# Optimization experiments

Measured on AMD Instinct MI355X. Metric: run time of the kernel, lower is better.

The kernel has to match this reference:

```python
import jax, jax.numpy as jnp
import numpy as np
import math

EPS = jnp.float32(1.1920929e-07)      # torch.finfo(torch.float).eps
FMIN = jnp.finfo(jnp.float32).min     # torch.finfo(torch.float).min
NEG = jnp.float32(-1e9)


def setup_inputs() -> dict:
    key = jax.random.key(0)
    ks = jax.random.split(key, 9)
    bs, l, sub, tgt, hidden, t_vocab, voc = 16, 1024, 2, 256, 512, 2000, 3000
    return {
        "out_logits": jax.random.normal(ks[0], (bs, tgt, t_vocab), jnp.float32),
        "feature": jax.random.normal(ks[1], (bs, tgt, hidden), jnp.float32),
        "memory_raw": jax.random.normal(ks[2], (bs, l, hidden), jnp.float32),
        "content_e": jax.random.randint(ks[3], (bs, l * sub), 0, voc, jnp.int64
                                        if jax.config.jax_enable_x64 else jnp.int32),
        "Wq": jax.random.normal(ks[4], (hidden, hidden), jnp.float32) * 0.02,
        "bq": jax.random.normal(ks[5], (hidden,), jnp.float32) * 0.02,
        "Wk": jax.random.normal(ks[6], (hidden, hidden * sub), jnp.float32) * 0.02,
        "bk": jax.random.normal(ks[7], (hidden * sub,), jnp.float32) * 0.02,
        "sentinel": jax.random.uniform(ks[8], (1, hidden), jnp.float32),
        "voc_len": 3000,
    }


def reference(out_logits, feature, memory_raw, content_e, Wq, bq, Wk, bk, sentinel, voc_len):
    bs, l, hidden = memory_raw.shape
    tgt_len = feature.shape[1]
    subtokens = Wk.shape[1] // hidden
    src_len = l * subtokens

    # decode(): out = log_softmax(prob(feature)); key_linear + subtoken expansion
    out = jax.nn.log_softmax(out_logits, axis=-1)                     # (bs, t, t_vocab)
    memory = (memory_raw @ Wk + bk).reshape(bs, src_len, hidden)      # (bs, s, h)
    key_padding_mask = content_e == 0                                 # (bs, s)

    # pointer(): attention over memory + sentinel
    pointer_key = jnp.concatenate(
        [memory, jnp.broadcast_to(sentinel[None, :, :], (bs, 1, hidden))], axis=1)
    pointer_query = jax.nn.gelu(feature @ Wq + bq, approximate=False) # (bs, t, h)
    atten = jnp.einsum('bth,bsh->bts', pointer_query, pointer_key) / math.sqrt(hidden)

    mask = jnp.concatenate(
        [key_padding_mask, jnp.zeros((bs, 1), bool)], axis=-1)[:, None, :]
    atten = jnp.where(mask, NEG, atten)
    atten = jax.nn.log_softmax(atten, axis=-1)                        # (bs, t, s+1)

    pointer_gate = atten[:, :, -1:]                                   # (bs, t, 1)
    exp_atten = jnp.exp(atten[:, :, :-1])                             # (bs, t, s)

    # scatter-add over src positions by extended-vocab id (== one-hot M einsum)
    def scat(ea_b, ce_b):  # ea_b: (t, s)  ce_b: (s,)
        return jax.ops.segment_sum(ea_b.T, ce_b, num_segments=voc_len).T  # (t, voc)
    pointer_atten_p = jax.vmap(scat)(exp_atten, content_e)            # (bs, t, voc)

    pointer_atten_log = jnp.log(pointer_atten_p + EPS)
    pointer_atten_log = pointer_atten_log - jnp.log1p(-jnp.exp(pointer_gate) + EPS)
    pointer_atten_log = jnp.where(jnp.isneginf(pointer_atten_log), FMIN, pointer_atten_log)

    pad = jnp.full((bs, tgt_len, voc_len - out.shape[-1]), -jnp.inf, jnp.float32)
    out = jnp.concatenate([out, pad], axis=-1)                        # (bs, t, voc)

    p = jnp.stack([out + pointer_gate,
                   pointer_atten_log + jnp.log(1.0 - jnp.exp(pointer_gate) + EPS)],
                  axis=-2)                                            # (bs, t, 2, voc)
    return jax.scipy.special.logsumexp(p, axis=-2)                    # (bs, t, voc)
```

## Files before the change

### kernel.cpp

```cpp
#include <hip/hip_runtime.h>
#include <math.h>

#define BSZ   16
#define LSEQ  1024
#define TGT   256
#define HID   512
#define TV    2000
#define VOC   3000
#define SRC   2048
#define NKE   1280
#define JOFF  640
#define CTILE 256
#define SCALE 0.044194173824159216f

typedef unsigned short u16;
typedef __attribute__((ext_vector_type(8))) short bf16x8;
typedef __attribute__((ext_vector_type(4))) float f32x4;

__device__ __forceinline__ u16 f2bf(float x) {
    unsigned u = __float_as_uint(x);
    u += 0x7FFFu + ((u >> 16) & 1u);
    return (u16)(u >> 16);
}
__device__ __forceinline__ float bf2f(u16 x) {
    return __uint_as_float((unsigned)x << 16);
}

static __device__ __forceinline__ float gelu_exact(float x) {
    return 0.5f * x * (1.0f + erff(x * 0.70710678118654752f));
}

__device__ __forceinline__ void gload16(const u16* g, u16* l) {
    __builtin_amdgcn_global_load_lds(
        (const __attribute__((address_space(1))) unsigned int*)g,
        (__attribute__((address_space(3))) unsigned int*)l,
        16, 0, 0);
}

__device__ __forceinline__ void cast8_body(const float4* __restrict__ in,
                                           int4* __restrict__ out, int i) {
    float4 x = in[2 * i], y = in[2 * i + 1];
    unsigned p0 = (unsigned)f2bf(x.x) | ((unsigned)f2bf(x.y) << 16);
    unsigned p1 = (unsigned)f2bf(x.z) | ((unsigned)f2bf(x.w) << 16);
    unsigned p2 = (unsigned)f2bf(y.x) | ((unsigned)f2bf(y.y) << 16);
    unsigned p3 = (unsigned)f2bf(y.z) | ((unsigned)f2bf(y.w) << 16);
    out[i] = make_int4(p0, p1, p2, p3);
}

__global__ __launch_bounds__(256) void prep_a(
    const float* __restrict__ feature, const float* __restrict__ Wq,
    const float* __restrict__ Wk, const float* __restrict__ sentinel,
    const float* __restrict__ bk,
    int4* __restrict__ featb, u16* __restrict__ wqT, u16* __restrict__ wkE,
    float* __restrict__ rowsum)
{
    __shared__ float t[32][33];
    const int id = blockIdx.x;
    const int tid = threadIdx.x;
    if (id < 1024) {
        cast8_body((const float4*)feature, featb, id * 256 + tid);
    } else if (id < 1280) {
        int id2 = id - 1024;
        int bx = (id2 & 15) * 32, by = (id2 >> 4) * 32;
        const int tx = tid & 31, ty = tid >> 5;
        #pragma unroll
        for (int k = 0; k < 4; ++k)
            t[ty + 8 * k][tx] = Wq[(size_t)(by + ty + 8 * k) * 512 + bx + tx];
        __syncthreads();
        #pragma unroll
        for (int k = 0; k < 4; ++k)
            wqT[(size_t)(bx + ty + 8 * k) * 512 + by + tx] = f2bf(t[tx][ty + 8 * k]);
    } else if (id < 1600) {
        const int rr = (id - 1280) * 4 + (tid >> 6);
        const int c = (tid & 63) * 8;
        const int j = rr >= JOFF;
        const int dd = rr - j * JOFF;
        u16* dst = wkE + (size_t)rr * HID + c;
        if (dd < 512) {
            const float* src = Wk + (size_t)dd * 1024 + j * 512 + c;
            #pragma unroll
            for (int k = 0; k < 8; ++k) dst[k] = f2bf(src[k]);
        } else if (dd == 512) {
            #pragma unroll
            for (int k = 0; k < 8; ++k) dst[k] = f2bf(sentinel[c + k]);
        } else if (dd == 513) {
            #pragma unroll
            for (int k = 0; k < 8; ++k) dst[k] = f2bf(bk[j * 512 + c + k]);
        } else {
            #pragma unroll
            for (int k = 0; k < 8; ++k) dst[k] = 0;
        }
    } else {
        float4* rz = (float4*)rowsum;
        for (int i = tid; i < 1024; i += 256) rz[i] = make_float4(0.f, 0.f, 0.f, 0.f);
    }
}

__global__ __launch_bounds__(256) void k_query(
    const u16* __restrict__ feat, const u16* __restrict__ wqT,
    const float* __restrict__ bq, u16* __restrict__ queryb,
    const float* __restrict__ memory_raw, int4* __restrict__ memb)
{
    __shared__ u16 sbuf[2 * 2048 * 2];
    const int id = blockIdx.x;
    const int tid = threadIdx.x;
    if (id >= 512) {
        cast8_body((const float4*)memory_raw, memb, (id - 512) * 256 + tid);
        return;
    }
    u16* As = sbuf;
    u16* Bs = sbuf + 2 * 2048;
    const int lane = tid & 63;
    const int w = tid >> 6;
    const int wr = (w >> 1) * 32, wc = (w & 1) * 32;
    const int m0 = (id >> 3) * 64, n0 = (id & 7) * 64;

    const int srow = tid >> 2, scol = (tid & 3) * 8;
    const u16* gA = feat + (size_t)(m0 + srow) * HID + scol;
    const u16* gB = wqT + (size_t)(n0 + srow) * HID + scol;

    const int la = lane & 15, lb = lane >> 4;
    f32x4 acc[2][2] = {};

    gload16(gA, As + w * 512);
    gload16(gB, Bs + w * 512);

    int cur = 0;
    for (int k0 = 0; k0 < HID; k0 += 32) {
        __syncthreads();
        const u16* Asb = As + cur * 2048;
        const u16* Bsb = Bs + cur * 2048;
        bf16x8 af[2], bf[2];
        #pragma unroll
        for (int i = 0; i < 2; ++i)
            af[i] = *(const bf16x8*)(Asb + (wr + i * 16 + la) * 32 + lb * 8);
        #pragma unroll
        for (int j = 0; j < 2; ++j)
            bf[j] = *(const bf16x8*)(Bsb + (wc + j * 16 + la) * 32 + lb * 8);
        if (k0 + 32 < HID) {
            const int nb = cur ^ 1;
            gload16(gA + k0 + 32, As + nb * 2048 + w * 512);
            gload16(gB + k0 + 32, Bs + nb * 2048 + w * 512);
        }
        #pragma unroll
        for (int i = 0; i < 2; ++i)
            #pragma unroll
            for (int j = 0; j < 2; ++j)
                acc[i][j] = __builtin_amdgcn_mfma_f32_16x16x32_bf16(af[i], bf[j], acc[i][j], 0, 0, 0);
        cur ^= 1;
    }

    const int r_l = (lane >> 4) * 4, c_l = lane & 15;
    #pragma unroll
    for (int j = 0; j < 2; ++j) {
        const int n = n0 + wc + j * 16 + c_l;
        const float bv = bq[n];
        #pragma unroll
        for (int i = 0; i < 2; ++i)
            #pragma unroll
            for (int r = 0; r < 4; ++r) {
                const int m = m0 + wr + i * 16 + r_l + r;
                queryb[(size_t)m * HID + n] = f2bf(gelu_exact(acc[i][j][r] + bv));
            }
    }
}

template<int EPI, int LDA, int LDB>
__device__ __forceinline__ void gemm_body(
    int m0, int n0, int z,
    const u16* __restrict__ Abase, const u16* __restrict__ Bbase,
    u16* __restrict__ outb,
    const int* __restrict__ ce, float* __restrict__ rowsum,
    u16* __restrict__ As, u16* __restrict__ Bs)
{
    const int tid = threadIdx.x;
    const int lane = tid & 63;
    const int w = tid >> 6;
    const int wr = (w >> 1) * 64, wc = (w & 1) * 64;

    const u16* Ag = Abase;
    const u16* Bg = Bbase;
    if (EPI == 2) {
        Ag = Abase + (size_t)(z >> 1) * LSEQ * HID;
        Bg = Bbase + (size_t)(z >> 1) * TGT * NKE + (size_t)(z & 1) * JOFF;
    }

    const int chunkrow = lane >> 2;
    const int colc = (lane & 3) * 8;
    const int c0 = w * 2, c1 = c0 + 1;
    const u16* gA0 = Ag + (size_t)(m0 + c0 * 16 + chunkrow) * LDA + colc;
    const u16* gA1 = Ag + (size_t)(m0 + c1 * 16 + chunkrow) * LDA + colc;
    const u16* gB0 = Bg + (size_t)(n0 + c0 * 16 + chunkrow) * LDB + colc;
    const u16* gB1 = Bg + (size_t)(n0 + c1 * 16 + chunkrow) * LDB + colc;

    const int la = lane & 15, lb = lane >> 4;
    f32x4 acc[4][4] = {};

    gload16(gA0, As + c0 * 512);
    gload16(gA1, As + c1 * 512);
    gload16(gB0, Bs + c0 * 512);
    gload16(gB1, Bs + c1 * 512);

    int cur = 0;
    for (int k0 = 0; k0 < HID; k0 += 32) {
        __syncthreads();
        const u16* Asb = As + cur * 4096;
        const u16* Bsb = Bs + cur * 4096;
        bf16x8 af[4], bfv[4];
        #pragma unroll
        for (int i = 0; i < 4; ++i)
            af[i] = *(const bf16x8*)(Asb + (wr + i * 16 + la) * 32 + lb * 8);
        #pragma unroll
        for (int j = 0; j < 4; ++j)
            bfv[j] = *(const bf16x8*)(Bsb + (wc + j * 16 + la) * 32 + lb * 8);
        if (k0 + 32 < HID) {
            const int nb = cur ^ 1;
            u16* An = As + nb * 4096;
            u16* Bn = Bs + nb * 4096;
            gload16(gA0 + k0 + 32, An + c0 * 512);
            gload16(gA1 + k0 + 32, An + c1 * 512);
            gload16(gB0 + k0 + 32, Bn + c0 * 512);
            gload16(gB1 + k0 + 32, Bn + c1 * 512);
        }
        #pragma unroll
        for (int i = 0; i < 4; ++i)
            #pragma unroll
            for (int j = 0; j < 4; ++j)
                acc[i][j] = __builtin_amdgcn_mfma_f32_16x16x32_bf16(af[i], bfv[j], acc[i][j], 0, 0, 0);
        cur ^= 1;
    }

    const int r_l = (lane >> 4) * 4, c_l = lane & 15;
    if (EPI == 3) {
        #pragma unroll
        for (int j = 0; j < 4; ++j) {
            const int n = n0 + wc + j * 16 + c_l;
            #pragma unroll
            for (int i = 0; i < 4; ++i)
                #pragma unroll
                for (int r = 0; r < 4; ++r) {
                    const int m = m0 + wr + i * 16 + r_l + r;
                    outb[(size_t)m * NKE + n] = f2bf(acc[i][j][r]);
                }
        }
    } else {
        const int b = z >> 1, jj = z & 1;
        float biasc[4];
        #pragma unroll
        for (int j = 0; j < 4; ++j) {
            const int n = n0 + wc + j * 16 + c_l;
            biasc[j] = bf2f(Bbase[(size_t)(b * TGT + n) * NKE + jj * JOFF + 513]);
        }
        const int* ceb = ce + (size_t)b * SRC;
        float csum[4] = {0.f, 0.f, 0.f, 0.f};
        #pragma unroll
        for (int i = 0; i < 4; ++i)
            #pragma unroll
            for (int r = 0; r < 4; ++r) {
                const int m = m0 + wr + i * 16 + r_l + r;
                const int cm = ceb[2 * m + jj];
                const size_t rowbase = ((size_t)b * SRC + jj * 1024 + m) * TGT;
                #pragma unroll
                for (int j = 0; j < 4; ++j) {
                    float ev = (cm == 0) ? 0.f
                             : __expf((acc[i][j][r] + biasc[j]) * SCALE);
                    outb[rowbase + n0 + wc + j * 16 + c_l] = f2bf(ev);
                    csum[j] += ev;
                }
            }
        #pragma unroll
        for (int j = 0; j < 4; ++j) {
            csum[j] += __shfl_xor(csum[j], 16, 64);
            csum[j] += __shfl_xor(csum[j], 32, 64);
        }
        const int jsel = lane >> 4;
        float myv = (jsel == 0) ? csum[0] : (jsel == 1) ? csum[1]
                  : (jsel == 2) ? csum[2] : csum[3];
        atomicAdd(&rowsum[b * TGT + n0 + wc + jsel * 16 + c_l], myv);
    }
}

__global__ __launch_bounds__(256) void k_qk(
    const u16* __restrict__ queryb, const u16* __restrict__ wkE,
    u16* __restrict__ qkb,
    const float* __restrict__ logits, float* __restrict__ lse,
    const int* __restrict__ ce, int* __restrict__ boff, u16* __restrict__ bucket)
{
    __shared__ u16 sbuf[4 * 4096];
    const int id = blockIdx.x;
    const int tid = threadIdx.x;
    if (id < 320) {
        gemm_body<3, 512, 512>((id / 10) * 128, (id % 10) * 128, 0,
                               queryb, wkE, qkb, nullptr, nullptr,
                               sbuf, sbuf + 2 * 4096);
    } else if (id < 1344) {
        const int row = (id - 320) * 4 + (tid >> 6);
        const int lane = tid & 63;
        const float4* lrow4 = (const float4*)(logits + (size_t)row * TV);
        float4 v4[8];
        float m = -INFINITY;
        #pragma unroll
        for (int k = 0; k < 8; ++k) {
            int idx = lane + 64 * k;
            if (idx < 500) {
                v4[k] = lrow4[idx];
                m = fmaxf(m, fmaxf(fmaxf(v4[k].x, v4[k].y), fmaxf(v4[k].z, v4[k].w)));
            } else {
                v4[k] = make_float4(-INFINITY, -INFINITY, -INFINITY, -INFINITY);
            }
        }
        #pragma unroll
        for (int o = 32; o > 0; o >>= 1) m = fmaxf(m, __shfl_xor(m, o, 64));
        float s = 0.f;
        #pragma unroll
        for (int k = 0; k < 8; ++k)
            s += __expf(v4[k].x - m) + __expf(v4[k].y - m)
               + __expf(v4[k].z - m) + __expf(v4[k].w - m);
        #pragma unroll
        for (int o = 32; o > 0; o >>= 1) s += __shfl_xor(s, o, 64);
        if (lane == 0) lse[row] = m + __logf(s);
    } else {
        const int b = id - 1344;
        int* cnt = (int*)sbuf;
        int* part = cnt + VOC;
        const int* ceb = ce + (size_t)b * SRC;
        for (int v = tid; v < VOC; v += 256) cnt[v] = 0;
        __syncthreads();
        for (int s = tid; s < SRC; s += 256) atomicAdd(&cnt[ceb[s]], 1);
        __syncthreads();
        const int base = tid * 12;
        int lc[12];
        int tot = 0;
        #pragma unroll
        for (int k = 0; k < 12; ++k) {
            int v = base + k;
            lc[k] = (v < VOC) ? cnt[v] : 0;
            tot += lc[k];
        }
        part[tid] = tot;
        __syncthreads();
        for (int d = 1; d < 256; d <<= 1) {
            int val = (tid >= d) ? part[tid - d] : 0;
            __syncthreads();
            part[tid] += val;
            __syncthreads();
        }
        int run = part[tid] - tot;
        int* boffb = boff + b * 3008;
        #pragma unroll
        for (int k = 0; k < 12; ++k) {
            int v = base + k;
            if (v < VOC) { boffb[v] = run; cnt[v] = run; run += lc[k]; }
        }
        if (tid == 0) boffb[VOC] = SRC;
        __syncthreads();
        for (int s = tid; s < SRC; s += 256) {
            int idv = ceb[s];
            int jl = (s & 1) * 1024 + (s >> 1);
            int pos = atomicAdd(&cnt[idv], 1);
            bucket[(size_t)b * SRC + pos] = (u16)jl;
        }
    }
}

__global__ __launch_bounds__(256) void gemm_atten(
    const u16* __restrict__ memb, const u16* __restrict__ qkb,
    const int* __restrict__ ce, float* __restrict__ rowsum,
    u16* __restrict__ etb)
{
    __shared__ u16 As[2 * 4096];
    __shared__ u16 Bs[2 * 4096];
    const int i = blockIdx.x;
    const int xcd = i & 7, slot = i >> 3;
    const int bjj = xcd + 8 * (slot >> 4);
    const int inner = slot & 15;
    gemm_body<2, 512, NKE>((inner >> 1) * 128, (inner & 1) * 128, bjj,
                           memb, qkb, etb, ce, rowsum, As, Bs);
}

__global__ __launch_bounds__(256) void combine(
    const u16* __restrict__ etb, const u16* __restrict__ bucket,
    const int* __restrict__ boff, const u16* __restrict__ qkb,
    const float* __restrict__ rowsum, const float* __restrict__ lse,
    const float* __restrict__ out_logits, float* __restrict__ out)
{
    __shared__ float part[CTILE][9];
    __shared__ float acc[8][256];
    __shared__ float rcInv[8], rcGZ[8], rcEdl[8], rcDl[8];
    const int i = blockIdx.x;
    const int xcd = i & 7, slot = i >> 3;
    const int b = xcd + 8 * (slot / 384);
    const int inner = slot % 384;
    const int tc = inner / 12, vs = inner % 12;
    const int t0 = tc * 8;
    const int vbase = vs * 256;
    const int tid = threadIdx.x;
    const float EPSF = 1.1920929e-07f;

    if (tid < 8) {
        const int bt = b * TGT + t0 + tid;
        const float sent_v = bf2f(qkb[(size_t)bt * NKE + 512]) * SCALE;
        const float se = __expf(sent_v);
        const float sm = rowsum[bt] + se;
        const float inv = 1.0f / sm;
        const float g = sent_v - __logf(sm);
        const float eg = se * inv;
        const float dl = __logf(1.0f - eg + EPSF) - log1pf(-eg + EPSF);
        rcInv[tid] = inv;
        rcGZ[tid] = g - lse[bt];
        rcEdl[tid] = __expf(dl);
        rcDl[tid] = dl;
    }

    const int* boffb = boff + b * 3008;
    const u16* bukb = bucket + (size_t)b * SRC;
    const u16* etbb = etb + (size_t)b * SRC * TGT;

    const int vend = (vbase + 256 < VOC) ? vbase + 256 : VOC;
    const int e_lo = boffb[vbase];
    const int cnt = boffb[vend] - e_lo;
    const int v = vbase + tid;
    const int i0 = (v < VOC) ? boffb[v] - e_lo : 0;
    const int i1 = (v < VOC) ? boffb[v + 1] - e_lo : 0;

    float a[8] = {0.f, 0.f, 0.f, 0.f, 0.f, 0.f, 0.f, 0.f};
    for (int ts = 0; ts < cnt; ts += CTILE) {
        const int n = (cnt - ts < CTILE) ? cnt - ts : CTILE;
        __syncthreads();
        for (int e = tid; e < n; e += 256) {
            const int s = bukb[e_lo + ts + e];
            int4 u = *(const int4*)(etbb + (size_t)s * TGT + t0);
            part[e][0] = bf2f((u16)(u.x & 0xffff));
            part[e][1] = bf2f((u16)((unsigned)u.x >> 16));
            part[e][2] = bf2f((u16)(u.y & 0xffff));
            part[e][3] = bf2f((u16)((unsigned)u.y >> 16));
            part[e][4] = bf2f((u16)(u.z & 0xffff));
            part[e][5] = bf2f((u16)((unsigned)u.z >> 16));
            part[e][6] = bf2f((u16)(u.w & 0xffff));
            part[e][7] = bf2f((u16)((unsigned)u.w >> 16));
        }
        __syncthreads();
        int lo = i0 - ts; if (lo < 0) lo = 0;
        int hi = i1 - ts; if (hi > n) hi = n;
        for (int e = lo; e < hi; ++e) {
            #pragma unroll
            for (int k = 0; k < 8; ++k) a[k] += part[e][k];
        }
    }
    #pragma unroll
    for (int k = 0; k < 8; ++k) acc[k][tid] = a[k];
    __syncthreads();

    const int r = tid >> 5;
    const int vl0 = tid & 31;
    const int bt = b * TGT + t0 + r;
    const float inv = rcInv[r], gZ = rcGZ[r], edl = rcEdl[r], dlv = rcDl[r];
    const float* lrow = out_logits + (size_t)bt * TV;
    float* orow = out + (size_t)bt * VOC;
    #pragma unroll
    for (int kk = 0; kk < 8; ++kk) {
        const int vloc = vl0 + 32 * kk;
        const int vv = vbase + vloc;
        if (vv >= VOC) continue;
        float pv = acc[r][vloc] * inv + EPSF;
        float o;
        if (vv < TV) o = __logf(__expf(lrow[vv] + gZ) + pv * edl);
        else         o = __logf(pv) + dlv;
        orow[vv] = o;
    }
}

extern "C" void kernel_launch(void* const* d_in, const int* in_sizes, int n_in,
                              void* d_out, int out_size, void* d_ws, size_t ws_size,
                              hipStream_t stream) {
    const float* out_logits = (const float*)d_in[0];
    const float* feature    = (const float*)d_in[1];
    const float* memory_raw = (const float*)d_in[2];
    const int*   content_e  = (const int*)d_in[3];
    const float* Wq = (const float*)d_in[4];
    const float* bq = (const float*)d_in[5];
    const float* Wk = (const float*)d_in[6];
    const float* bk = (const float*)d_in[7];
    const float* sentinel = (const float*)d_in[8];
    float* out = (float*)d_out;

    u16* memb   = (u16*)d_ws;
    u16* featb  = memb   + (size_t)16384 * 512;
    u16* wqT    = featb  + (size_t)4096 * 512;
    u16* wkE    = wqT    + (size_t)512 * 512;
    u16* queryb = wkE    + (size_t)NKE * 512;
    u16* qkb    = queryb + (size_t)4096 * 512;
    u16* etb    = qkb    + (size_t)4096 * NKE;
    float* rowsum = (float*)(etb + (size_t)BSZ * SRC * TGT);
    float* lse   = rowsum + 4096;
    int* boff = (int*)(lse + 4096);
    u16* bucket = (u16*)(boff + 16 * 3008);

    prep_a<<<1601, 256, 0, stream>>>(feature, Wq, Wk, sentinel, bk,
                                     (int4*)featb, wqT, wkE, rowsum);
    k_query<<<4608, 256, 0, stream>>>(featb, wqT, bq, queryb, memory_raw, (int4*)memb);
    k_qk<<<1360, 256, 0, stream>>>(queryb, wkE, qkb, out_logits, lse,
                                   content_e, boff, bucket);
    gemm_atten<<<512, 256, 0, stream>>>(memb, qkb, content_e, rowsum, etb);
    combine<<<6144, 256, 0, stream>>>(etb, bucket, boff, qkb,
                                      rowsum, lse, out_logits, out);
}
```

Baseline: 89.62 us.

## Rebalance side work across kernels: bucketing into prep, LSE into attention GEMM

Moves the per-batch content-id bucketing (histogram, scan, scatter) into the first prep kernel and the logits log-sum-exp rows into the attention GEMM launch. k_qk becomes a pure 320-block GEMM. The aim is to fill idle CUs during the small qk GEMM and the 512-block attention GEMM with independent work, at the cost of prep_a now reserving about 13KB of extra LDS in every block and a heavier attention launch.

Result: no change. 91.05 us (+1.6%).

```diff
diff --git a/kernel.cpp b/kernel.cpp
--- a/kernel.cpp
+++ b/kernel.cpp
@@ -50,11 +50,13 @@
 __global__ __launch_bounds__(256) void prep_a(
     const float* __restrict__ feature, const float* __restrict__ Wq,
     const float* __restrict__ Wk, const float* __restrict__ sentinel,
-    const float* __restrict__ bk,
+    const float* __restrict__ bk, const int* __restrict__ ce,
     int4* __restrict__ featb, u16* __restrict__ wqT, u16* __restrict__ wkE,
-    float* __restrict__ rowsum)
+    float* __restrict__ rowsum, int* __restrict__ boff, u16* __restrict__ bucket)
 {
     __shared__ float t[32][33];
+    __shared__ int cnt[VOC];
+    __shared__ int part[256];
     const int id = blockIdx.x;
     const int tid = threadIdx.x;
     if (id < 1024) {
@@ -90,9 +92,48 @@
             #pragma unroll
             for (int k = 0; k < 8; ++k) dst[k] = 0;
         }
-    } else {
+    } else if (id == 1600) {
         float4* rz = (float4*)rowsum;
         for (int i = tid; i < 1024; i += 256) rz[i] = make_float4(0.f, 0.f, 0.f, 0.f);
+    } else {
+        const int b = id - 1601;
+        const int* ceb = ce + (size_t)b * SRC;
+        for (int v = tid; v < VOC; v += 256) cnt[v] = 0;
+        __syncthreads();
+        for (int s = tid; s < SRC; s += 256) atomicAdd(&cnt[ceb[s]], 1);
+        __syncthreads();
+        const int base = tid * 12;
+        int lc[12];
+        int tot = 0;
+        #pragma unroll
+        for (int k = 0; k < 12; ++k) {
+            int v = base + k;
+            lc[k] = (v < VOC) ? cnt[v] : 0;
+            tot += lc[k];
+        }
+        part[tid] = tot;
+        __syncthreads();
+        for (int d = 1; d < 256; d <<= 1) {
+            int val = (tid >= d) ? part[tid - d] : 0;
+            __syncthreads();
+            part[tid] += val;
+            __syncthreads();
+        }
+        int run = part[tid] - tot;
+        int* boffb = boff + b * 3008;
+        #pragma unroll
+        for (int k = 0; k < 12; ++k) {
+            int v = base + k;
+            if (v < VOC) { boffb[v] = run; cnt[v] = run; run += lc[k]; }
+        }
+        if (tid == 0) boffb[VOC] = SRC;
+        __syncthreads();
+        for (int s = tid; s < SRC; s += 256) {
+            int idv = ceb[s];
+            int jl = (s & 1) * 1024 + (s >> 1);
+            int pos = atomicAdd(&cnt[idv], 1);
+            bucket[(size_t)b * SRC + pos] = (u16)jl;
+        }
     }
 }
 
@@ -282,19 +323,33 @@
 
 __global__ __launch_bounds__(256) void k_qk(
     const u16* __restrict__ queryb, const u16* __restrict__ wkE,
-    u16* __restrict__ qkb,
-    const float* __restrict__ logits, float* __restrict__ lse,
-    const int* __restrict__ ce, int* __restrict__ boff, u16* __restrict__ bucket)
+    u16* __restrict__ qkb)
 {
-    __shared__ u16 sbuf[4 * 4096];
+    __shared__ u16 As[2 * 4096];
+    __shared__ u16 Bs[2 * 4096];
     const int id = blockIdx.x;
+    gemm_body<3, 512, 512>((id / 10) * 128, (id % 10) * 128, 0,
+                           queryb, wkE, qkb, nullptr, nullptr, As, Bs);
+}
+
+__global__ __launch_bounds__(256) void k_atten(
+    const u16* __restrict__ memb, const u16* __restrict__ qkb,
+    const int* __restrict__ ce, float* __restrict__ rowsum,
+    u16* __restrict__ etb,
+    const float* __restrict__ logits, float* __restrict__ lse)
+{
+    __shared__ u16 As[2 * 4096];
+    __shared__ u16 Bs[2 * 4096];
+    const int i = blockIdx.x;
     const int tid = threadIdx.x;
-    if (id < 320) {
-        gemm_body<3, 512, 512>((id / 10) * 128, (id % 10) * 128, 0,
-                               queryb, wkE, qkb, nullptr, nullptr,
-                               sbuf, sbuf + 2 * 4096);
-    } else if (id < 1344) {
-        const int row = (id - 320) * 4 + (tid >> 6);
+    if (i < 512) {
+        const int xcd = i & 7, slot = i >> 3;
+        const int bjj = xcd + 8 * (slot >> 4);
+        const int inner = slot & 15;
+        gemm_body<2, 512, NKE>((inner >> 1) * 128, (inner & 1) * 128, bjj,
+                               memb, qkb, etb, ce, rowsum, As, Bs);
+    } else {
+        const int row = (i - 512) * 4 + (tid >> 6);
         const int lane = tid & 63;
         const float4* lrow4 = (const float4*)(logits + (size_t)row * TV);
         float4 v4[8];
@@ -319,63 +374,7 @@
         #pragma unroll
         for (int o = 32; o > 0; o >>= 1) s += __shfl_xor(s, o, 64);
         if (lane == 0) lse[row] = m + __logf(s);
-    } else {
-        const int b = id - 1344;
-        int* cnt = (int*)sbuf;
-        int* part = cnt + VOC;
-        const int* ceb = ce + (size_t)b * SRC;
-        for (int v = tid; v < VOC; v += 256) cnt[v] = 0;
-        __syncthreads();
-        for (int s = tid; s < SRC; s += 256) atomicAdd(&cnt[ceb[s]], 1);
-        __syncthreads();
-        const int base = tid * 12;
-        int lc[12];
-        int tot = 0;
-        #pragma unroll
-        for (int k = 0; k < 12; ++k) {
-            int v = base + k;
-            lc[k] = (v < VOC) ? cnt[v] : 0;
-            tot += lc[k];
-        }
-        part[tid] = tot;
-        __syncthreads();
-        for (int d = 1; d < 256; d <<= 1) {
-            int val = (tid >= d) ? part[tid - d] : 0;
-            __syncthreads();
-            part[tid] += val;
-            __syncthreads();
-        }
-        int run = part[tid] - tot;
-        int* boffb = boff + b * 3008;
-        #pragma unroll
-        for (int k = 0; k < 12; ++k) {
-            int v = base + k;
-            if (v < VOC) { boffb[v] = run; cnt[v] = run; run += lc[k]; }
-        }
-        if (tid == 0) boffb[VOC] = SRC;
-        __syncthreads();
-        for (int s = tid; s < SRC; s += 256) {
-            int idv = ceb[s];
-            int jl = (s & 1) * 1024 + (s >> 1);
-            int pos = atomicAdd(&cnt[idv], 1);
-            bucket[(size_t)b * SRC + pos] = (u16)jl;
-        }
-    }
-}
-
-__global__ __launch_bounds__(256) void gemm_atten(
-    const u16* __restrict__ memb, const u16* __restrict__ qkb,
-    const int* __restrict__ ce, float* __restrict__ rowsum,
-    u16* __restrict__ etb)
-{
-    __shared__ u16 As[2 * 4096];
-    __shared__ u16 Bs[2 * 4096];
-    const int i = blockIdx.x;
-    const int xcd = i & 7, slot = i >> 3;
-    const int bjj = xcd + 8 * (slot >> 4);
-    const int inner = slot & 15;
-    gemm_body<2, 512, NKE>((inner >> 1) * 128, (inner & 1) * 128, bjj,
-                           memb, qkb, etb, ce, rowsum, As, Bs);
+    }
 }
 
 __global__ __launch_bounds__(256) void combine(
@@ -496,12 +495,12 @@
     int* boff = (int*)(lse + 4096);
     u16* bucket = (u16*)(boff + 16 * 3008);
 
-    prep_a<<<1601, 256, 0, stream>>>(feature, Wq, Wk, sentinel, bk,
-                                     (int4*)featb, wqT, wkE, rowsum);
+    prep_a<<<1617, 256, 0, stream>>>(feature, Wq, Wk, sentinel, bk, content_e,
+                                     (int4*)featb, wqT, wkE, rowsum, boff, bucket);
     k_query<<<4608, 256, 0, stream>>>(featb, wqT, bq, queryb, memory_raw, (int4*)memb);
-    k_qk<<<1360, 256, 0, stream>>>(queryb, wkE, qkb, out_logits, lse,
-                                   content_e, boff, bucket);
-    gemm_atten<<<512, 256, 0, stream>>>(memb, qkb, content_e, rowsum, etb);
+    k_qk<<<320, 256, 0, stream>>>(queryb, wkE, qkb);
+    k_atten<<<1536, 256, 0, stream>>>(memb, qkb, content_e, rowsum, etb,
+                                      out_logits, lse);
     combine<<<6144, 256, 0, stream>>>(etb, bucket, boff, qkb,
                                       rowsum, lse, out_logits, out);
 }
```
